# Performance work log

Hardware: AMD Instinct MI355X
Metric: run time of the kernel (lower is better)

The kernel has to match this reference:

```python
import jax, jax.numpy as jnp
import numpy as np

B, N, D, E, K, C = 64, 32, 384, 8, 8, 1000  # batch, tokens, dim, experts, capacity, classes
KD = K * D   # expert_dims = 3072
ND = N * D   # 12288

def _gelu(v):
    return jax.nn.gelu(v, approximate=False)  # torch nn.GELU default = exact erf

def setup_inputs() -> dict:
    key = jax.random.key(0)
    ks = jax.random.split(key, 16)
    s = 0.02
    f = jnp.float32
    return {
        "x": jax.random.normal(ks[0], (B, N, D), f),
        "expert_emb": jax.random.normal(ks[1], (E, D), f) * s,
        "w1": jax.random.normal(ks[2], (E, KD, KD), f) * s,
        "b1": jnp.zeros((E, KD), f),
        "w2": jax.random.normal(ks[3], (E, KD, KD), f) * s,
        "b2": jnp.zeros((E, KD), f),
        "sw_w1": jax.random.normal(ks[4], (ND, ND), f) * s,
        "sw_b1": jnp.zeros((ND,), f),
        "sw_w2": jax.random.normal(ks[5], (ND, E), f) * s,
        "sw_b2": jnp.zeros((E,), f),
        "ch_w1": jax.random.normal(ks[6], (KD, KD), f) * s,
        "ch_b1": jnp.zeros((KD,), f),
        "ch_w2": jax.random.normal(ks[7], (KD, C), f) * s,
        "ch_b2": jnp.zeros((C,), f),
    }

def reference(x, expert_emb, w1, b1, w2, b2, sw_w1, sw_b1, sw_w2, sw_b2, ch_w1, ch_b1, ch_w2, ch_b2):
    # Router: scores (B, E, N), softmax over tokens, expert-choice top-k
    S = jax.nn.softmax(jnp.einsum('bnd,ed->ben', x, expert_emb), axis=2)
    G, I = jax.lax.top_k(S, K)  # (B, E, K); G is unused downstream (matches original)
    # Gather selected tokens per expert: (B, E, K, D)
    sel = x[jnp.arange(B)[:, None, None], I]
    sel = jnp.transpose(sel, (1, 0, 2, 3)).reshape(E, B, KD)  # e b (k d)
    # Per-expert MLP as grouped GEMM
    h = _gelu(jnp.einsum('ebi,eio->ebo', sel, w1) + b1[:, None, :])
    er = jnp.einsum('ebi,eio->ebo', h, w2) + b2[:, None, :]   # (E, B, KD)
    er = jnp.transpose(er, (1, 0, 2))                          # (B, E, KD)
    # Weighted combine: weights from Mlp over flattened input + softmax over experts
    xf = x.reshape(B, ND)
    w = jax.nn.softmax(_gelu(xf @ sw_w1 + sw_b1) @ sw_w2 + sw_b2, axis=1)  # (B, E)
    ws = jnp.einsum('bek,be->bk', er, w)                       # (B, KD)
    # Classification head
    return _gelu(ws @ ch_w1 + ch_b1) @ ch_w2 + ch_b2           # (B, C)
```

## Files before the change

### kernel.cpp

```cpp
#include <hip/hip_runtime.h>
#include <hip/hip_bf16.h>

using short8 = __attribute__((ext_vector_type(8))) short;
using f32x4  = __attribute__((ext_vector_type(4))) float;

typedef const __attribute__((address_space(1))) void* gvp;
typedef __attribute__((address_space(3))) void* lvp;

#define NB   64
#define NTOK 32
#define DD   384
#define NE   8
#define TK   8
#define NC   1000
#define KD   3072
#define ND   12288

__device__ __forceinline__ float gelu_f(float x) {
  return 0.5f * x * (1.0f + erff(x * 0.70710678118654752440f));
}

__device__ __forceinline__ unsigned short f2bf(float f) {
  unsigned u = __float_as_uint(f);
  u += 0x7fffu + ((u >> 16) & 1u);
  return (unsigned short)(u >> 16);
}

__global__ __launch_bounds__(256) void routing_kernel(
    const float* __restrict__ x, const float* __restrict__ emb,
    unsigned short* __restrict__ sel, unsigned short* __restrict__ xb)
{
  __shared__ float xs[NTOK][DD + 1];
  __shared__ float es[NE][DD + 1];
  __shared__ float lg[NE][NTOK];
  __shared__ int   Is[NE][TK];
  const int b = blockIdx.x, tid = threadIdx.x;

  for (int i = tid; i < NTOK * DD; i += 256) xs[i / DD][i % DD] = x[(size_t)b * ND + i];
  for (int i = tid; i < NE * DD;   i += 256) es[i / DD][i % DD] = emb[i];
  __syncthreads();

  {
    const int e = tid >> 5, n = tid & 31;
    float s = 0.f;
    for (int d = 0; d < DD; ++d) s += xs[n][d] * es[e][d];
    lg[e][n] = s;
  }
  __syncthreads();

  if (tid < NE) {
    const int e = tid;
    for (int k = 0; k < TK; ++k) {
      float best = lg[e][0]; int bi = 0;
      for (int n = 1; n < NTOK; ++n) { float v = lg[e][n]; if (v > best) { best = v; bi = n; } }
      Is[e][k] = bi;
      lg[e][bi] = -INFINITY;
    }
  }
  __syncthreads();

  for (int i = tid; i < NE * KD; i += 256) {
    const int e = i / KD, r = i % KD, k = r / DD, d = r % DD;
    const int n = Is[e][k];
    sel[((size_t)e * NB + b) * KD + r] = f2bf(xs[n][d]);
  }
  for (int i = tid; i < ND; i += 256) xb[(size_t)b * ND + i] = f2bf(xs[i / DD][i % DD]);
}

template<int K, int N, int SPLIT, bool NGUARD>
__global__ __launch_bounds__(256) void gemm2(
    const unsigned short* __restrict__ A, const float* __restrict__ W,
    float* __restrict__ outp, const int nbatch)
{
  constexpr int KCH = K / SPLIT;
  constexpr int NSTEP = KCH / 32;
  __shared__ float lw[2][4096];

  const int t = threadIdx.x;
  const int wv = t >> 6, lane = t & 63;
  const int n0 = blockIdx.x * 128;
  const int bt = blockIdx.y, z = blockIdx.z;

  const unsigned short* Ab = A + (size_t)bt * 64 * K + (size_t)z * KCH;
  const float*          Wb = W + (size_t)bt * (size_t)K * N;

  const int srow = wv * 8 + (lane >> 5);
  const int scol = (((lane & 31) * 4) - wv * 8) & 127;
  const float* gsrc   = Wb + (size_t)(z * KCH + srow) * N + n0 + scol;
  const float* glimit = Wb + (size_t)K * N - 4;
  float* lbase = &lw[0][0] + wv * 1024 + lane * 4;

  auto stage = [&](int bf, int st) {
    const float* g = gsrc + (size_t)st * 32 * N;
    float* l = lbase + bf * 4096;
    #pragma unroll
    for (int r = 0; r < 4; ++r) {
      const float* gp = g + r * 2 * N;
      if (NGUARD && gp > glimit) gp = glimit;
      __builtin_amdgcn_global_load_lds((gvp)gp, (lvp)(l + r * 256), 16, 0, 0);
    }
  };

  const int ln = lane & 15, q = lane >> 4, g8 = q * 8;
  const int colp0 = (wv * 32 +      ln + g8) & 127;
  const int colp1 = (wv * 32 + 16 + ln + g8) & 127;
  const unsigned short* ap = Ab + (size_t)ln * K + g8;

  f32x4 acc[4][2];
  #pragma unroll
  for (int mt = 0; mt < 4; ++mt) {
    acc[mt][0] = (f32x4){0.f, 0.f, 0.f, 0.f};
    acc[mt][1] = (f32x4){0.f, 0.f, 0.f, 0.f};
  }

  stage(0, 0);
  for (int st = 0; st < NSTEP; ++st) {
    const int bf = st & 1;
    __syncthreads();
    if (st + 1 < NSTEP) stage(bf ^ 1, st + 1);

    const float* lb = &lw[bf][0];
    union { short8 v; unsigned short u[8]; } pb0, pb1;
    #pragma unroll
    for (int j = 0; j < 8; ++j) {
      pb0.u[j] = f2bf(lb[(g8 + j) * 128 + colp0]);
      pb1.u[j] = f2bf(lb[(g8 + j) * 128 + colp1]);
    }
    #pragma unroll
    for (int mt = 0; mt < 4; ++mt) {
      const short8 afr = *reinterpret_cast<const short8*>(ap + (size_t)mt * 16 * K + st * 32);
      acc[mt][0] = __builtin_amdgcn_mfma_f32_16x16x32_bf16(afr, pb0.v, acc[mt][0], 0, 0, 0);
      acc[mt][1] = __builtin_amdgcn_mfma_f32_16x16x32_bf16(afr, pb1.v, acc[mt][1], 0, 0, 0);
    }
  }

  float* op = outp + (size_t)(z * nbatch + bt) * 64 * N;
  #pragma unroll
  for (int mt = 0; mt < 4; ++mt)
    #pragma unroll
    for (int s = 0; s < 2; ++s) {
      const int col = n0 + wv * 32 + s * 16 + ln;
      if (NGUARD && col >= N) continue;
      #pragma unroll
      for (int r = 0; r < 4; ++r) {
        const int m = mt * 16 + q * 4 + r;
        op[(size_t)m * N + col] = acc[mt][s][r];
      }
    }
}

template<int SPLIT, bool GELU, bool OUTBF>
__global__ __launch_bounds__(256) void reduce_ep(
    const float* __restrict__ part, const float* __restrict__ bias,
    void* __restrict__ outv, const int N, const int nbatch)
{
  const int total = nbatch * 64 * N;
  const int idx = blockIdx.x * 256 + threadIdx.x;
  if (idx >= total) return;
  const int n = idx % N;
  const int bt = idx / (64 * N);
  float s = 0.f;
  #pragma unroll
  for (int zz = 0; zz < SPLIT; ++zz) s += part[(size_t)zz * total + idx];
  s += bias[(size_t)bt * N + n];
  if (GELU) s = gelu_f(s);
  if (OUTBF) ((unsigned short*)outv)[idx] = f2bf(s);
  else       ((float*)outv)[idx] = s;
}

__global__ __launch_bounds__(256) void swgate_kernel(
    const float* __restrict__ t, const float* __restrict__ w2,
    const float* __restrict__ b2, float* __restrict__ wout)
{
  __shared__ float red[256][8];
  __shared__ float lg[8];
  const int b = blockIdx.x, tid = threadIdx.x;
  float p0=0,p1=0,p2=0,p3=0,p4=0,p5=0,p6=0,p7=0;
  const float* tb = t + (size_t)b * ND;
  for (int i = tid; i < ND; i += 256) {
    const float tv = tb[i];
    const float4* wp = reinterpret_cast<const float4*>(w2 + (size_t)i * 8);
    const float4 wa = wp[0], wc = wp[1];
    p0 += tv * wa.x; p1 += tv * wa.y; p2 += tv * wa.z; p3 += tv * wa.w;
    p4 += tv * wc.x; p5 += tv * wc.y; p6 += tv * wc.z; p7 += tv * wc.w;
  }
  red[tid][0]=p0; red[tid][1]=p1; red[tid][2]=p2; red[tid][3]=p3;
  red[tid][4]=p4; red[tid][5]=p5; red[tid][6]=p6; red[tid][7]=p7;
  __syncthreads();
  if (tid < 8) {
    float s = 0.f;
    for (int i = 0; i < 256; ++i) s += red[i][tid];
    lg[tid] = s + b2[tid];
  }
  __syncthreads();
  if (tid == 0) {
    float mx = lg[0];
    for (int e = 1; e < 8; ++e) mx = fmaxf(mx, lg[e]);
    float sum = 0.f;
    for (int e = 0; e < 8; ++e) sum += expf(lg[e] - mx);
    for (int e = 0; e < 8; ++e) wout[b * 8 + e] = expf(lg[e] - mx) / sum;
  }
}

__global__ __launch_bounds__(256) void mix2_kernel(
    const float* __restrict__ part, const float* __restrict__ b2,
    const float* __restrict__ wv, unsigned short* __restrict__ wsb)
{
  const int idx = blockIdx.x * 256 + threadIdx.x;
  const int b = idx / KD, c = idx % KD;
  float s = 0.f;
  #pragma unroll
  for (int e = 0; e < NE; ++e) {
    float v = b2[(size_t)e * KD + c];
    #pragma unroll
    for (int zz = 0; zz < 4; ++zz)
      v += part[((size_t)(zz * NE + e) * NB + b) * KD + c];
    s += v * wv[b * NE + e];
  }
  wsb[idx] = f2bf(s);
}

extern "C" void kernel_launch(void* const* d_in, const int* in_sizes, int n_in,
                              void* d_out, int out_size, void* d_ws, size_t ws_size,
                              hipStream_t stream)
{
  (void)in_sizes; (void)n_in; (void)out_size; (void)ws_size;
  const float* x     = (const float*)d_in[0];
  const float* emb   = (const float*)d_in[1];
  const float* w1    = (const float*)d_in[2];
  const float* b1    = (const float*)d_in[3];
  const float* w2    = (const float*)d_in[4];
  const float* b2    = (const float*)d_in[5];
  const float* sw_w1 = (const float*)d_in[6];
  const float* sw_b1 = (const float*)d_in[7];
  const float* sw_w2 = (const float*)d_in[8];
  const float* sw_b2 = (const float*)d_in[9];
  const float* ch_w1 = (const float*)d_in[10];
  const float* ch_b1 = (const float*)d_in[11];
  const float* ch_w2 = (const float*)d_in[12];
  const float* ch_b2 = (const float*)d_in[13];
  float* out = (float*)d_out;

  char* ws = (char*)d_ws;
  size_t off = 0;
  auto alloc = [&](size_t bytes) -> void* {
    void* p = ws + off;
    off += (bytes + 255) & ~(size_t)255;
    return p;
  };
  unsigned short* sel  = (unsigned short*)alloc((size_t)NE * NB * KD * 2);
  unsigned short* xb   = (unsigned short*)alloc((size_t)NB * ND * 2);
  unsigned short* h    = (unsigned short*)alloc((size_t)NE * NB * KD * 2);
  float*          ep   = (float*)alloc((size_t)4 * NE * NB * KD * 4);
  float*          tpt  = (float*)alloc((size_t)8 * NB * ND * 4);
  float*          tt   = (float*)alloc((size_t)NB * ND * 4);
  float*          wv   = (float*)alloc((size_t)NB * NE * 4);
  unsigned short* wsb  = (unsigned short*)alloc((size_t)NB * KD * 2);
  float*          g1p  = (float*)alloc((size_t)16 * NB * KD * 4);
  unsigned short* g1   = (unsigned short*)alloc((size_t)NB * KD * 2);
  float*          g2p  = (float*)alloc((size_t)32 * NB * NC * 4);

  routing_kernel<<<dim3(64), 256, 0, stream>>>(x, emb, sel, xb);
  gemm2<KD, KD, 4, false><<<dim3(24, 8, 4), 256, 0, stream>>>(sel, w1, ep, 8);
  reduce_ep<4, true, true><<<dim3(6144), 256, 0, stream>>>(ep, b1, (void*)h, KD, 8);
  gemm2<KD, KD, 4, false><<<dim3(24, 8, 4), 256, 0, stream>>>(h, w2, ep, 8);
  gemm2<ND, ND, 8, false><<<dim3(96, 1, 8), 256, 0, stream>>>(xb, sw_w1, tpt, 1);
  reduce_ep<8, true, false><<<dim3(3072), 256, 0, stream>>>(tpt, sw_b1, (void*)tt, ND, 1);
  swgate_kernel<<<dim3(64), 256, 0, stream>>>(tt, sw_w2, sw_b2, wv);
  mix2_kernel<<<dim3((NB * KD) / 256), 256, 0, stream>>>(ep, b2, wv, wsb);
  gemm2<KD, KD, 16, false><<<dim3(24, 1, 16), 256, 0, stream>>>(wsb, ch_w1, g1p, 1);
  reduce_ep<16, true, true><<<dim3(768), 256, 0, stream>>>(g1p, ch_b1, (void*)g1, KD, 1);
  gemm2<KD, NC, 32, true><<<dim3(8, 1, 32), 256, 0, stream>>>(g1, ch_w2, g2p, 1);
  reduce_ep<32, false, false><<<dim3((NB * NC + 255) / 256), 256, 0, stream>>>(g2p, ch_b2, (void*)out, NC, 1);
}
```

Measured before the change: 380.3 us.

## Widen GEMM N-tile to 256, halve split-K, fuse sw reduce into gate

```diff
diff --git a/kernel.cpp b/kernel.cpp
--- a/kernel.cpp
+++ b/kernel.cpp
@@ -68,50 +68,49 @@
 }
 
 template<int K, int N, int SPLIT, bool NGUARD>
-__global__ __launch_bounds__(256) void gemm2(
+__global__ __launch_bounds__(256) void gemm3(
     const unsigned short* __restrict__ A, const float* __restrict__ W,
     float* __restrict__ outp, const int nbatch)
 {
   constexpr int KCH = K / SPLIT;
   constexpr int NSTEP = KCH / 32;
-  __shared__ float lw[2][4096];
+  __shared__ float lw[2][8192];
 
   const int t = threadIdx.x;
   const int wv = t >> 6, lane = t & 63;
-  const int n0 = blockIdx.x * 128;
+  const int n0 = blockIdx.x * 256;
   const int bt = blockIdx.y, z = blockIdx.z;
 
   const unsigned short* Ab = A + (size_t)bt * 64 * K + (size_t)z * KCH;
   const float*          Wb = W + (size_t)bt * (size_t)K * N;
 
-  const int srow = wv * 8 + (lane >> 5);
-  const int scol = (((lane & 31) * 4) - wv * 8) & 127;
-  const float* gsrc   = Wb + (size_t)(z * KCH + srow) * N + n0 + scol;
+  const int scol = ((lane * 4) - wv * 8) & 255;
+  const float* gsrc   = Wb + (size_t)(z * KCH + wv * 8) * N + n0 + scol;
   const float* glimit = Wb + (size_t)K * N - 4;
-  float* lbase = &lw[0][0] + wv * 1024 + lane * 4;
+  float* lbase = &lw[0][0] + (wv * 8) * 256 + lane * 4;
 
   auto stage = [&](int bf, int st) {
     const float* g = gsrc + (size_t)st * 32 * N;
-    float* l = lbase + bf * 4096;
-    #pragma unroll
-    for (int r = 0; r < 4; ++r) {
-      const float* gp = g + r * 2 * N;
+    float* l = lbase + bf * 8192;
+    #pragma unroll
+    for (int r = 0; r < 8; ++r) {
+      const float* gp = g + (size_t)r * N;
       if (NGUARD && gp > glimit) gp = glimit;
       __builtin_amdgcn_global_load_lds((gvp)gp, (lvp)(l + r * 256), 16, 0, 0);
     }
   };
 
   const int ln = lane & 15, q = lane >> 4, g8 = q * 8;
-  const int colp0 = (wv * 32 +      ln + g8) & 127;
-  const int colp1 = (wv * 32 + 16 + ln + g8) & 127;
   const unsigned short* ap = Ab + (size_t)ln * K + g8;
-
-  f32x4 acc[4][2];
-  #pragma unroll
-  for (int mt = 0; mt < 4; ++mt) {
-    acc[mt][0] = (f32x4){0.f, 0.f, 0.f, 0.f};
-    acc[mt][1] = (f32x4){0.f, 0.f, 0.f, 0.f};
-  }
+  int colp[4];
+  #pragma unroll
+  for (int s = 0; s < 4; ++s) colp[s] = (wv * 64 + s * 16 + ln + 8 * q) & 255;
+
+  f32x4 acc[4][4];
+  #pragma unroll
+  for (int mt = 0; mt < 4; ++mt)
+    #pragma unroll
+    for (int s = 0; s < 4; ++s) acc[mt][s] = (f32x4){0.f, 0.f, 0.f, 0.f};
 
   stage(0, 0);
   for (int st = 0; st < NSTEP; ++st) {
@@ -120,32 +119,35 @@
     if (st + 1 < NSTEP) stage(bf ^ 1, st + 1);
 
     const float* lb = &lw[bf][0];
-    union { short8 v; unsigned short u[8]; } pb0, pb1;
-    #pragma unroll
-    for (int j = 0; j < 8; ++j) {
-      pb0.u[j] = f2bf(lb[(g8 + j) * 128 + colp0]);
-      pb1.u[j] = f2bf(lb[(g8 + j) * 128 + colp1]);
-    }
-    #pragma unroll
-    for (int mt = 0; mt < 4; ++mt) {
-      const short8 afr = *reinterpret_cast<const short8*>(ap + (size_t)mt * 16 * K + st * 32);
-      acc[mt][0] = __builtin_amdgcn_mfma_f32_16x16x32_bf16(afr, pb0.v, acc[mt][0], 0, 0, 0);
-      acc[mt][1] = __builtin_amdgcn_mfma_f32_16x16x32_bf16(afr, pb1.v, acc[mt][1], 0, 0, 0);
-    }
+    union { short8 v; unsigned short u[8]; } pb[4];
+    #pragma unroll
+    for (int s = 0; s < 4; ++s)
+      #pragma unroll
+      for (int j = 0; j < 8; ++j)
+        pb[s].u[j] = f2bf(lb[(g8 + j) * 256 + colp[s]]);
+
+    short8 afr[4];
+    #pragma unroll
+    for (int mt = 0; mt < 4; ++mt)
+      afr[mt] = *reinterpret_cast<const short8*>(ap + (size_t)mt * 16 * K + st * 32);
+
+    #pragma unroll
+    for (int mt = 0; mt < 4; ++mt)
+      #pragma unroll
+      for (int s = 0; s < 4; ++s)
+        acc[mt][s] = __builtin_amdgcn_mfma_f32_16x16x32_bf16(afr[mt], pb[s].v, acc[mt][s], 0, 0, 0);
   }
 
   float* op = outp + (size_t)(z * nbatch + bt) * 64 * N;
   #pragma unroll
   for (int mt = 0; mt < 4; ++mt)
     #pragma unroll
-    for (int s = 0; s < 2; ++s) {
-      const int col = n0 + wv * 32 + s * 16 + ln;
+    for (int s = 0; s < 4; ++s) {
+      const int col = n0 + wv * 64 + s * 16 + ln;
       if (NGUARD && col >= N) continue;
       #pragma unroll
-      for (int r = 0; r < 4; ++r) {
-        const int m = mt * 16 + q * 4 + r;
-        op[(size_t)m * N + col] = acc[mt][s][r];
-      }
+      for (int r = 0; r < 4; ++r)
+        op[(size_t)(mt * 16 + q * 4 + r) * N + col] = acc[mt][s][r];
     }
 }
 
@@ -168,40 +170,52 @@
   else       ((float*)outv)[idx] = s;
 }
 
-__global__ __launch_bounds__(256) void swgate_kernel(
-    const float* __restrict__ t, const float* __restrict__ w2,
-    const float* __restrict__ b2, float* __restrict__ wout)
+template<int SPLIT>
+__global__ __launch_bounds__(256) void swgate2_kernel(
+    const float* __restrict__ part, const float* __restrict__ b1,
+    const float* __restrict__ w2, const float* __restrict__ b2,
+    float* __restrict__ wout)
 {
   __shared__ float red[256][8];
-  __shared__ float lg[8];
   const int b = blockIdx.x, tid = threadIdx.x;
-  float p0=0,p1=0,p2=0,p3=0,p4=0,p5=0,p6=0,p7=0;
-  const float* tb = t + (size_t)b * ND;
+  float p[8] = {0, 0, 0, 0, 0, 0, 0, 0};
   for (int i = tid; i < ND; i += 256) {
-    const float tv = tb[i];
+    float tv = b1[i];
+    #pragma unroll
+    for (int zz = 0; zz < SPLIT; ++zz)
+      tv += part[(size_t)zz * (64 * ND) + (size_t)b * ND + i];
+    tv = gelu_f(tv);
     const float4* wp = reinterpret_cast<const float4*>(w2 + (size_t)i * 8);
     const float4 wa = wp[0], wc = wp[1];
-    p0 += tv * wa.x; p1 += tv * wa.y; p2 += tv * wa.z; p3 += tv * wa.w;
-    p4 += tv * wc.x; p5 += tv * wc.y; p6 += tv * wc.z; p7 += tv * wc.w;
-  }
-  red[tid][0]=p0; red[tid][1]=p1; red[tid][2]=p2; red[tid][3]=p3;
-  red[tid][4]=p4; red[tid][5]=p5; red[tid][6]=p6; red[tid][7]=p7;
-  __syncthreads();
-  if (tid < 8) {
-    float s = 0.f;
-    for (int i = 0; i < 256; ++i) s += red[i][tid];
-    lg[tid] = s + b2[tid];
-  }
-  __syncthreads();
+    p[0] += tv * wa.x; p[1] += tv * wa.y; p[2] += tv * wa.z; p[3] += tv * wa.w;
+    p[4] += tv * wc.x; p[5] += tv * wc.y; p[6] += tv * wc.z; p[7] += tv * wc.w;
+  }
+  #pragma unroll
+  for (int e = 0; e < 8; ++e) red[tid][e] = p[e];
+  __syncthreads();
+  for (int off = 128; off >= 1; off >>= 1) {
+    if (tid < off) {
+      #pragma unroll
+      for (int e = 0; e < 8; ++e) red[tid][e] += red[tid + off][e];
+    }
+    __syncthreads();
+  }
   if (tid == 0) {
+    float lg[8];
+    #pragma unroll
+    for (int e = 0; e < 8; ++e) lg[e] = red[0][e] + b2[e];
     float mx = lg[0];
+    #pragma unroll
     for (int e = 1; e < 8; ++e) mx = fmaxf(mx, lg[e]);
     float sum = 0.f;
+    #pragma unroll
     for (int e = 0; e < 8; ++e) sum += expf(lg[e] - mx);
+    #pragma unroll
     for (int e = 0; e < 8; ++e) wout[b * 8 + e] = expf(lg[e] - mx) / sum;
   }
 }
 
+template<int SPLIT>
 __global__ __launch_bounds__(256) void mix2_kernel(
     const float* __restrict__ part, const float* __restrict__ b2,
     const float* __restrict__ wv, unsigned short* __restrict__ wsb)
@@ -213,7 +227,7 @@
   for (int e = 0; e < NE; ++e) {
     float v = b2[(size_t)e * KD + c];
     #pragma unroll
-    for (int zz = 0; zz < 4; ++zz)
+    for (int zz = 0; zz < SPLIT; ++zz)
       v += part[((size_t)(zz * NE + e) * NB + b) * KD + c];
     s += v * wv[b * NE + e];
   }
@@ -251,9 +265,8 @@
   unsigned short* sel  = (unsigned short*)alloc((size_t)NE * NB * KD * 2);
   unsigned short* xb   = (unsigned short*)alloc((size_t)NB * ND * 2);
   unsigned short* h    = (unsigned short*)alloc((size_t)NE * NB * KD * 2);
-  float*          ep   = (float*)alloc((size_t)4 * NE * NB * KD * 4);
-  float*          tpt  = (float*)alloc((size_t)8 * NB * ND * 4);
-  float*          tt   = (float*)alloc((size_t)NB * ND * 4);
+  float*          ep   = (float*)alloc((size_t)2 * NE * NB * KD * 4);
+  float*          tpt  = (float*)alloc((size_t)4 * NB * ND * 4);
   float*          wv   = (float*)alloc((size_t)NB * NE * 4);
   unsigned short* wsb  = (unsigned short*)alloc((size_t)NB * KD * 2);
   float*          g1p  = (float*)alloc((size_t)16 * NB * KD * 4);
@@ -261,15 +274,14 @@
   float*          g2p  = (float*)alloc((size_t)32 * NB * NC * 4);
 
   routing_kernel<<<dim3(64), 256, 0, stream>>>(x, emb, sel, xb);
-  gemm2<KD, KD, 4, false><<<dim3(24, 8, 4), 256, 0, stream>>>(sel, w1, ep, 8);
-  reduce_ep<4, true, true><<<dim3(6144), 256, 0, stream>>>(ep, b1, (void*)h, KD, 8);
-  gemm2<KD, KD, 4, false><<<dim3(24, 8, 4), 256, 0, stream>>>(h, w2, ep, 8);
-  gemm2<ND, ND, 8, false><<<dim3(96, 1, 8), 256, 0, stream>>>(xb, sw_w1, tpt, 1);
-  reduce_ep<8, true, false><<<dim3(3072), 256, 0, stream>>>(tpt, sw_b1, (void*)tt, ND, 1);
-  swgate_kernel<<<dim3(64), 256, 0, stream>>>(tt, sw_w2, sw_b2, wv);
-  mix2_kernel<<<dim3((NB * KD) / 256), 256, 0, stream>>>(ep, b2, wv, wsb);
-  gemm2<KD, KD, 16, false><<<dim3(24, 1, 16), 256, 0, stream>>>(wsb, ch_w1, g1p, 1);
+  gemm3<KD, KD, 2, false><<<dim3(12, 8, 2), 256, 0, stream>>>(sel, w1, ep, 8);
+  reduce_ep<2, true, true><<<dim3(6144), 256, 0, stream>>>(ep, b1, (void*)h, KD, 8);
+  gemm3<KD, KD, 2, false><<<dim3(12, 8, 2), 256, 0, stream>>>(h, w2, ep, 8);
+  gemm3<ND, ND, 4, false><<<dim3(48, 1, 4), 256, 0, stream>>>(xb, sw_w1, tpt, 1);
+  swgate2_kernel<4><<<dim3(64), 256, 0, stream>>>(tpt, sw_b1, sw_w2, sw_b2, wv);
+  mix2_kernel<2><<<dim3((NB * KD) / 256), 256, 0, stream>>>(ep, b2, wv, wsb);
+  gemm3<KD, KD, 16, false><<<dim3(12, 1, 16), 256, 0, stream>>>(wsb, ch_w1, g1p, 1);
   reduce_ep<16, true, true><<<dim3(768), 256, 0, stream>>>(g1p, ch_b1, (void*)g1, KD, 1);
-  gemm2<KD, NC, 32, true><<<dim3(8, 1, 32), 256, 0, stream>>>(g1, ch_w2, g2p, 1);
+  gemm3<KD, NC, 32, true><<<dim3(4, 1, 32), 256, 0, stream>>>(g1, ch_w2, g2p, 1);
   reduce_ep<32, false, false><<<dim3((NB * NC + 255) / 256), 256, 0, stream>>>(g2p, ch_b2, (void*)out, NC, 1);
 }
```

Result: slower. 447.1 us (+17.6%).

## Co-schedule expert GEMMs with split switch-MLP GEMM and fuse gate reduction

Applied to the files above, without the earlier changes.

```diff
diff --git a/kernel.cpp b/kernel.cpp
--- a/kernel.cpp
+++ b/kernel.cpp
@@ -67,6 +67,100 @@
   for (int i = tid; i < ND; i += 256) xb[(size_t)b * ND + i] = f2bf(xs[i / DD][i % DD]);
 }
 
+__device__ __forceinline__ void gemm_rt_body(
+    const unsigned short* __restrict__ Ab, const float* __restrict__ Wz,
+    float* __restrict__ op, const int K, const int N, const int NSTEP,
+    const int n0, const int wv, const int lane, float* __restrict__ lw)
+{
+  const int srow = wv * 8 + (lane >> 5);
+  const int scol = (((lane & 31) * 4) - wv * 8) & 127;
+  const float* gsrc = Wz + (size_t)srow * N + n0 + scol;
+  float* lbase = lw + wv * 1024 + lane * 4;
+
+  auto stage = [&](int bf, int st) {
+    const float* g = gsrc + (size_t)st * 32 * N;
+    float* l = lbase + bf * 4096;
+    #pragma unroll
+    for (int r = 0; r < 4; ++r)
+      __builtin_amdgcn_global_load_lds((gvp)(g + (size_t)(r * 2) * N),
+                                       (lvp)(l + r * 256), 16, 0, 0);
+  };
+
+  const int ln = lane & 15, q = lane >> 4, g8 = q * 8;
+  const unsigned short* ap = Ab + (size_t)ln * K + g8;
+  const int colp0 = (wv * 32 +      ln + g8) & 127;
+  const int colp1 = (wv * 32 + 16 + ln + g8) & 127;
+
+  f32x4 acc[4][2];
+  #pragma unroll
+  for (int mt = 0; mt < 4; ++mt) {
+    acc[mt][0] = (f32x4){0.f, 0.f, 0.f, 0.f};
+    acc[mt][1] = (f32x4){0.f, 0.f, 0.f, 0.f};
+  }
+
+  stage(0, 0);
+  for (int st = 0; st < NSTEP; ++st) {
+    const int bf = st & 1;
+    __syncthreads();
+    if (st + 1 < NSTEP) stage(bf ^ 1, st + 1);
+
+    const float* lb = lw + bf * 4096;
+    union { short8 v; unsigned short u[8]; } pb0, pb1;
+    #pragma unroll
+    for (int j = 0; j < 8; ++j) {
+      pb0.u[j] = f2bf(lb[(g8 + j) * 128 + colp0]);
+      pb1.u[j] = f2bf(lb[(g8 + j) * 128 + colp1]);
+    }
+    #pragma unroll
+    for (int mt = 0; mt < 4; ++mt) {
+      const short8 afr = *reinterpret_cast<const short8*>(ap + (size_t)mt * 16 * K + st * 32);
+      acc[mt][0] = __builtin_amdgcn_mfma_f32_16x16x32_bf16(afr, pb0.v, acc[mt][0], 0, 0, 0);
+      acc[mt][1] = __builtin_amdgcn_mfma_f32_16x16x32_bf16(afr, pb1.v, acc[mt][1], 0, 0, 0);
+    }
+  }
+
+  #pragma unroll
+  for (int mt = 0; mt < 4; ++mt)
+    #pragma unroll
+    for (int s = 0; s < 2; ++s) {
+      const int col = n0 + wv * 32 + s * 16 + ln;
+      #pragma unroll
+      for (int r = 0; r < 4; ++r)
+        op[(size_t)(mt * 16 + q * 4 + r) * N + col] = acc[mt][s][r];
+    }
+}
+
+template<int PHASE>
+__global__ __launch_bounds__(256) void dual_gemm(
+    const unsigned short* __restrict__ EA, const float* __restrict__ EW,
+    float* __restrict__ EO,
+    const unsigned short* __restrict__ xb, const float* __restrict__ sww1,
+    float* __restrict__ tpt)
+{
+  __shared__ float lw[2][4096];
+  const int t = threadIdx.x, wv = t >> 6, lane = t & 63;
+  const int bid = blockIdx.x;
+  const int grp = bid / 3, rem = bid - grp * 3;
+
+  if (rem < 2) {
+    const int idx = grp * 2 + rem;
+    const int z = idx & 3, bt = (idx >> 2) & 7, nx = idx >> 5;
+    constexpr int KCH = KD / 4;
+    gemm_rt_body(EA + (size_t)bt * 64 * KD + (size_t)z * KCH,
+                 EW + (size_t)bt * KD * KD + (size_t)z * KCH * KD,
+                 EO + ((size_t)z * NE + bt) * 64 * KD,
+                 KD, KD, KCH / 32, nx * 128, wv, lane, &lw[0][0]);
+  } else {
+    const int idx = grp;
+    const int z = PHASE * 4 + (idx & 3), nx = idx >> 2;
+    constexpr int KCH = ND / 8;
+    gemm_rt_body(xb + (size_t)z * KCH,
+                 sww1 + (size_t)z * KCH * ND,
+                 tpt + (size_t)z * 64 * ND,
+                 ND, ND, KCH / 32, nx * 128, wv, lane, &lw[0][0]);
+  }
+}
+
 template<int K, int N, int SPLIT, bool NGUARD>
 __global__ __launch_bounds__(256) void gemm2(
     const unsigned short* __restrict__ A, const float* __restrict__ W,
@@ -95,16 +189,16 @@
     float* l = lbase + bf * 4096;
     #pragma unroll
     for (int r = 0; r < 4; ++r) {
-      const float* gp = g + r * 2 * N;
+      const float* gp = g + (size_t)(r * 2) * N;
       if (NGUARD && gp > glimit) gp = glimit;
       __builtin_amdgcn_global_load_lds((gvp)gp, (lvp)(l + r * 256), 16, 0, 0);
     }
   };
 
   const int ln = lane & 15, q = lane >> 4, g8 = q * 8;
+  const unsigned short* ap = Ab + (size_t)ln * K + g8;
   const int colp0 = (wv * 32 +      ln + g8) & 127;
   const int colp1 = (wv * 32 + 16 + ln + g8) & 127;
-  const unsigned short* ap = Ab + (size_t)ln * K + g8;
 
   f32x4 acc[4][2];
   #pragma unroll
@@ -142,10 +236,8 @@
       const int col = n0 + wv * 32 + s * 16 + ln;
       if (NGUARD && col >= N) continue;
       #pragma unroll
-      for (int r = 0; r < 4; ++r) {
-        const int m = mt * 16 + q * 4 + r;
-        op[(size_t)m * N + col] = acc[mt][s][r];
-      }
+      for (int r = 0; r < 4; ++r)
+        op[(size_t)(mt * 16 + q * 4 + r) * N + col] = acc[mt][s][r];
     }
 }
 
@@ -168,54 +260,73 @@
   else       ((float*)outv)[idx] = s;
 }
 
-__global__ __launch_bounds__(256) void swgate_kernel(
-    const float* __restrict__ t, const float* __restrict__ w2,
-    const float* __restrict__ b2, float* __restrict__ wout)
+__global__ __launch_bounds__(256) void sw1part_kernel(
+    const float* __restrict__ tpt, const float* __restrict__ b1,
+    const float* __restrict__ w2, float* __restrict__ pd)
 {
   __shared__ float red[256][8];
-  __shared__ float lg[8];
-  const int b = blockIdx.x, tid = threadIdx.x;
-  float p0=0,p1=0,p2=0,p3=0,p4=0,p5=0,p6=0,p7=0;
-  const float* tb = t + (size_t)b * ND;
-  for (int i = tid; i < ND; i += 256) {
-    const float tv = tb[i];
+  const int blk = blockIdx.x, tid = threadIdx.x;
+  const int b = blk / 12, sl = blk % 12;
+  const int base = sl * 1024;
+
+  float p[8] = {0, 0, 0, 0, 0, 0, 0, 0};
+  #pragma unroll
+  for (int k = 0; k < 4; ++k) {
+    const int i = base + k * 256 + tid;
+    float tv = b1[i];
+    #pragma unroll
+    for (int zz = 0; zz < 8; ++zz)
+      tv += tpt[(size_t)zz * (64 * ND) + (size_t)b * ND + i];
+    tv = gelu_f(tv);
     const float4* wp = reinterpret_cast<const float4*>(w2 + (size_t)i * 8);
     const float4 wa = wp[0], wc = wp[1];
-    p0 += tv * wa.x; p1 += tv * wa.y; p2 += tv * wa.z; p3 += tv * wa.w;
-    p4 += tv * wc.x; p5 += tv * wc.y; p6 += tv * wc.z; p7 += tv * wc.w;
-  }
-  red[tid][0]=p0; red[tid][1]=p1; red[tid][2]=p2; red[tid][3]=p3;
-  red[tid][4]=p4; red[tid][5]=p5; red[tid][6]=p6; red[tid][7]=p7;
+    p[0] += tv * wa.x; p[1] += tv * wa.y; p[2] += tv * wa.z; p[3] += tv * wa.w;
+    p[4] += tv * wc.x; p[5] += tv * wc.y; p[6] += tv * wc.z; p[7] += tv * wc.w;
+  }
+  #pragma unroll
+  for (int e = 0; e < 8; ++e) red[tid][e] = p[e];
   __syncthreads();
-  if (tid < 8) {
-    float s = 0.f;
-    for (int i = 0; i < 256; ++i) s += red[i][tid];
-    lg[tid] = s + b2[tid];
-  }
-  __syncthreads();
-  if (tid == 0) {
-    float mx = lg[0];
-    for (int e = 1; e < 8; ++e) mx = fmaxf(mx, lg[e]);
-    float sum = 0.f;
-    for (int e = 0; e < 8; ++e) sum += expf(lg[e] - mx);
-    for (int e = 0; e < 8; ++e) wout[b * 8 + e] = expf(lg[e] - mx) / sum;
-  }
-}
-
-__global__ __launch_bounds__(256) void mix2_kernel(
-    const float* __restrict__ part, const float* __restrict__ b2,
-    const float* __restrict__ wv, unsigned short* __restrict__ wsb)
+  for (int off = 128; off >= 1; off >>= 1) {
+    if (tid < off) {
+      #pragma unroll
+      for (int e = 0; e < 8; ++e) red[tid][e] += red[tid + off][e];
+    }
+    __syncthreads();
+  }
+  if (tid < 8) pd[(size_t)blk * 8 + tid] = red[0][tid];
+}
+
+__global__ __launch_bounds__(256) void mix2s_kernel(
+    const float* __restrict__ ep, const float* __restrict__ b2,
+    const float* __restrict__ pd, const float* __restrict__ swb2,
+    unsigned short* __restrict__ wsb)
 {
   const int idx = blockIdx.x * 256 + threadIdx.x;
   const int b = idx / KD, c = idx % KD;
+
+  float lg[8];
+  #pragma unroll
+  for (int e = 0; e < 8; ++e) lg[e] = swb2[e];
+  for (int sl = 0; sl < 12; ++sl)
+    #pragma unroll
+    for (int e = 0; e < 8; ++e) lg[e] += pd[((size_t)b * 12 + sl) * 8 + e];
+  float mx = lg[0];
+  #pragma unroll
+  for (int e = 1; e < 8; ++e) mx = fmaxf(mx, lg[e]);
+  float sum = 0.f;
+  float w[8];
+  #pragma unroll
+  for (int e = 0; e < 8; ++e) { w[e] = expf(lg[e] - mx); sum += w[e]; }
+  const float inv = 1.f / sum;
+
   float s = 0.f;
   #pragma unroll
   for (int e = 0; e < NE; ++e) {
     float v = b2[(size_t)e * KD + c];
     #pragma unroll
     for (int zz = 0; zz < 4; ++zz)
-      v += part[((size_t)(zz * NE + e) * NB + b) * KD + c];
-    s += v * wv[b * NE + e];
+      v += ep[((size_t)(zz * NE + e) * NB + b) * KD + c];
+    s += v * (w[e] * inv);
   }
   wsb[idx] = f2bf(s);
 }
@@ -253,21 +364,18 @@
   unsigned short* h    = (unsigned short*)alloc((size_t)NE * NB * KD * 2);
   float*          ep   = (float*)alloc((size_t)4 * NE * NB * KD * 4);
   float*          tpt  = (float*)alloc((size_t)8 * NB * ND * 4);
-  float*          tt   = (float*)alloc((size_t)NB * ND * 4);
-  float*          wv   = (float*)alloc((size_t)NB * NE * 4);
+  float*          pd   = (float*)alloc((size_t)NB * 12 * 8 * 4);
   unsigned short* wsb  = (unsigned short*)alloc((size_t)NB * KD * 2);
   float*          g1p  = (float*)alloc((size_t)16 * NB * KD * 4);
   unsigned short* g1   = (unsigned short*)alloc((size_t)NB * KD * 2);
   float*          g2p  = (float*)alloc((size_t)32 * NB * NC * 4);
 
   routing_kernel<<<dim3(64), 256, 0, stream>>>(x, emb, sel, xb);
-  gemm2<KD, KD, 4, false><<<dim3(24, 8, 4), 256, 0, stream>>>(sel, w1, ep, 8);
+  dual_gemm<0><<<dim3(1152), 256, 0, stream>>>(sel, w1, ep, xb, sw_w1, tpt);
   reduce_ep<4, true, true><<<dim3(6144), 256, 0, stream>>>(ep, b1, (void*)h, KD, 8);
-  gemm2<KD, KD, 4, false><<<dim3(24, 8, 4), 256, 0, stream>>>(h, w2, ep, 8);
-  gemm2<ND, ND, 8, false><<<dim3(96, 1, 8), 256, 0, stream>>>(xb, sw_w1, tpt, 1);
-  reduce_ep<8, true, false><<<dim3(3072), 256, 0, stream>>>(tpt, sw_b1, (void*)tt, ND, 1);
-  swgate_kernel<<<dim3(64), 256, 0, stream>>>(tt, sw_w2, sw_b2, wv);
-  mix2_kernel<<<dim3((NB * KD) / 256), 256, 0, stream>>>(ep, b2, wv, wsb);
+  dual_gemm<1><<<dim3(1152), 256, 0, stream>>>(h, w2, ep, xb, sw_w1, tpt);
+  sw1part_kernel<<<dim3(768), 256, 0, stream>>>(tpt, sw_b1, sw_w2, pd);
+  mix2s_kernel<<<dim3((NB * KD) / 256), 256, 0, stream>>>(ep, b2, pd, sw_b2, wsb);
   gemm2<KD, KD, 16, false><<<dim3(24, 1, 16), 256, 0, stream>>>(wsb, ch_w1, g1p, 1);
   reduce_ep<16, true, true><<<dim3(768), 256, 0, stream>>>(g1p, ch_b1, (void*)g1, KD, 1);
   gemm2<KD, NC, 32, true><<<dim3(8, 1, 32), 256, 0, stream>>>(g1, ch_w2, g2p, 1);
```

Result: slower. 405.3 us (+6.6%).
